# Kernel optimization log

Hardware: AMD Instinct MI355X
Metric: run time of the kernel (lower is better)

The kernel has to match this reference:

```python
import jax, jax.numpy as jnp
import numpy as np


def setup_inputs() -> dict:
    key = jax.random.key(0)
    k1, k2, k3, k4 = jax.random.split(key, 4)
    B, N, d_in, d_out = 8, 2048, 256, 256
    x = jax.random.normal(k1, (B, N, d_in), dtype=jnp.float32)
    adj_hat = jax.random.uniform(k2, (B, N, N), dtype=jnp.float32)
    W = jax.random.normal(k3, (d_out, d_in), dtype=jnp.float32) * (1.0 / np.sqrt(d_in))
    b = jax.random.normal(k4, (d_out,), dtype=jnp.float32) * 0.01
    return {"x": x, "adj_hat": adj_hat, "W": W, "b": b}


def reference(x, adj_hat, W, b):
    # Degrees from adj = adj_hat - I (i.e. without self loops): row sum minus diagonal.
    N = adj_hat.shape[1]
    diag = jnp.diagonal(adj_hat, axis1=-2, axis2=-1)          # [B, N]
    d = adj_hat.sum(axis=-1) - diag                           # [B, N]
    d_inv_sqrt = jnp.power(d, -0.5)                           # [B, N]
    # dad = D^-1/2 @ adj_hat @ D^-1/2  ==  d_i * a_ij * d_j (elementwise broadcast)
    dad = d_inv_sqrt[:, :, None] * adj_hat * d_inv_sqrt[:, None, :]  # [B, N, N]
    h = jnp.einsum('bnd,od->bno', x, W) + b                   # projection [B, N, d_out]
    return jnp.einsum('bnm,bmo->bno', dad, h)                 # [B, N, d_out]
```

## Files before the change

kernel.cpp:

```cpp
#include <hip/hip_runtime.h>
#include <hip/hip_bf16.h>


#define BATCH 8
#define NN    2048
#define DIN   256
#define DOUT  256
#define RTOT  (BATCH * NN)

typedef short  bf16x8  __attribute__((ext_vector_type(8)));
typedef short  short4v __attribute__((ext_vector_type(4)));
typedef float  f32x4   __attribute__((ext_vector_type(4)));

__device__ __forceinline__ short f2bf(float f) {
    union { float f; unsigned u; } v; v.f = f;
    unsigned r = v.u + 0x7fffu + ((v.u >> 16) & 1u);
    return (short)(r >> 16);
}

__global__ __launch_bounds__(256) void k_degree(const float* __restrict__ adj,
                                                float* __restrict__ dis) {
    int row = blockIdx.x;
    int b = row >> 11, n = row & (NN - 1);
    const float4* rp4 = (const float4*)(adj + ((size_t)b * NN + n) * NN);
    float s = 0.f;
#pragma unroll
    for (int i = 0; i < 2; i++) {
        float4 v = rp4[threadIdx.x + i * 256];
        s += (v.x + v.y) + (v.z + v.w);
    }
#pragma unroll
    for (int off = 32; off; off >>= 1) s += __shfl_down(s, off);
    __shared__ float red[4];
    if ((threadIdx.x & 63) == 0) red[threadIdx.x >> 6] = s;
    __syncthreads();
    if (threadIdx.x == 0) {
        float tot  = (red[0] + red[1]) + (red[2] + red[3]);
        float diag = ((const float*)rp4)[n];
        dis[row]   = rsqrtf(tot - diag);
    }
}

__global__ __launch_bounds__(256) void k_proj(const float* __restrict__ x,
                                              const float* __restrict__ W,
                                              const float* __restrict__ bias,
                                              const float* __restrict__ dis,
                                              unsigned short* __restrict__ hT) {
    const int mt  = blockIdx.y;
    const int nt  = blockIdx.x;
    const int tid = threadIdx.x;
    const int w = tid >> 6, lane = tid & 63;
    const int wr = w >> 1, wc = w & 1;
    const int l16 = lane & 15, quad = lane >> 4;

    __shared__ short As[128][32];
    __shared__ short Bs[128][32];

    f32x4 acc[4][4];
#pragma unroll
    for (int i = 0; i < 4; i++)
#pragma unroll
        for (int j = 0; j < 4; j++) acc[i][j] = (f32x4){0.f, 0.f, 0.f, 0.f};

    const float4* Wf4 = (const float4*)(W + (size_t)mt * 128 * DIN);
    const float4* Xf4 = (const float4*)(x + (size_t)nt * 128 * DIN);

    for (int kk = 0; kk < DIN / 32; kk++) {
        const int k0 = kk * 32;
        __syncthreads();
#pragma unroll
        for (int it = 0; it < 4; it++) {
            int idx = tid + it * 256;
            int r = idx >> 3, c = idx & 7;
            float4 va = Wf4[(size_t)r * (DIN / 4) + (k0 >> 2) + c];
            float4 vb = Xf4[(size_t)r * (DIN / 4) + (k0 >> 2) + c];
            short4v sa = { f2bf(va.x), f2bf(va.y), f2bf(va.z), f2bf(va.w) };
            short4v sb = { f2bf(vb.x), f2bf(vb.y), f2bf(vb.z), f2bf(vb.w) };
            *(short4v*)&As[r][c * 4] = sa;
            *(short4v*)&Bs[r][c * 4] = sb;
        }
        __syncthreads();
        bf16x8 af[4], bfv[4];
#pragma unroll
        for (int i = 0; i < 4; i++) af[i]  = *(bf16x8*)&As[wr * 64 + i * 16 + l16][quad * 8];
#pragma unroll
        for (int j = 0; j < 4; j++) bfv[j] = *(bf16x8*)&Bs[wc * 64 + j * 16 + l16][quad * 8];
#pragma unroll
        for (int i = 0; i < 4; i++)
#pragma unroll
            for (int j = 0; j < 4; j++)
                acc[i][j] = __builtin_amdgcn_mfma_f32_16x16x32_bf16(af[i], bfv[j], acc[i][j], 0, 0, 0);
    }

#pragma unroll
    for (int i = 0; i < 4; i++) {
        const int orow_base = mt * 128 + wr * 64 + i * 16 + quad * 4;
#pragma unroll
        for (int r = 0; r < 4; r++) {
            const int orow = orow_base + r;
            const float bb = bias[orow];
#pragma unroll
            for (int j = 0; j < 4; j++) {
                const int col = nt * 128 + wc * 64 + j * 16 + l16;
                float v = (acc[i][j][r] + bb) * dis[col];
                hT[(size_t)orow * RTOT + col] = (unsigned short)f2bf(v);
            }
        }
    }
}

__global__ __launch_bounds__(256) void k_main(const float* __restrict__ adj,
                                              const unsigned short* __restrict__ hT,
                                              const float* __restrict__ dis,
                                              float* __restrict__ out) {
    const int b     = blockIdx.x & 7;
    const int mtile = blockIdx.x >> 3;
    const int n0    = mtile * 64;
    const int tid = threadIdx.x;
    const int w = tid >> 6, lane = tid & 63;
    const int l16 = lane & 15, quad = lane >> 4;

    __shared__ short As[64][32];
    __shared__ short Bs[256][32];

    f32x4 acc[4][4];
#pragma unroll
    for (int i = 0; i < 4; i++)
#pragma unroll
        for (int j = 0; j < 4; j++) acc[i][j] = (f32x4){0.f, 0.f, 0.f, 0.f};

    const float4* adj4 = (const float4*)(adj + ((size_t)b * NN + n0) * NN);
    const unsigned short* hTb = hT + (size_t)b * NN;

    for (int kk = 0; kk < NN / 32; kk++) {
        const int k0 = kk * 32;
        __syncthreads();
#pragma unroll
        for (int it = 0; it < 2; it++) {
            int idx = tid + it * 256;
            int r = idx >> 3, c = idx & 7;
            float4 v = adj4[(size_t)r * (NN / 4) + (k0 >> 2) + c];
            short4v sv = { f2bf(v.x), f2bf(v.y), f2bf(v.z), f2bf(v.w) };
            *(short4v*)&As[r][c * 4] = sv;
        }
#pragma unroll
        for (int it = 0; it < 4; it++) {
            int idx = tid + it * 256;
            int o = idx >> 2, c = idx & 3;
            bf16x8 hv = *(const bf16x8*)(hTb + (size_t)o * RTOT + k0 + c * 8);
            *(bf16x8*)&Bs[o][c * 8] = hv;
        }
        __syncthreads();
        bf16x8 af[4], bfv[4];
#pragma unroll
        for (int i = 0; i < 4; i++) af[i]  = *(bf16x8*)&As[i * 16 + l16][quad * 8];
#pragma unroll
        for (int j = 0; j < 4; j++) bfv[j] = *(bf16x8*)&Bs[w * 64 + j * 16 + l16][quad * 8];
#pragma unroll
        for (int i = 0; i < 4; i++)
#pragma unroll
            for (int j = 0; j < 4; j++)
                acc[i][j] = __builtin_amdgcn_mfma_f32_16x16x32_bf16(af[i], bfv[j], acc[i][j], 0, 0, 0);
    }

    const float* disb = dis + (size_t)b * NN;
#pragma unroll
    for (int i = 0; i < 4; i++) {
#pragma unroll
        for (int r = 0; r < 4; r++) {
            const int nrow = n0 + i * 16 + quad * 4 + r;
            const float dn = disb[nrow];
#pragma unroll
            for (int j = 0; j < 4; j++) {
                const int ocol = w * 64 + j * 16 + l16;
                out[((size_t)b * NN + nrow) * DOUT + ocol] = dn * acc[i][j][r];
            }
        }
    }
}

extern "C" void kernel_launch(void* const* d_in, const int* in_sizes, int n_in,
                              void* d_out, int out_size, void* d_ws, size_t ws_size,
                              hipStream_t stream) {
    const float* x    = (const float*)d_in[0];
    const float* adj  = (const float*)d_in[1];
    const float* W    = (const float*)d_in[2];
    const float* bias = (const float*)d_in[3];
    float* out = (float*)d_out;

    float* dis = (float*)d_ws;
    unsigned short* hT = (unsigned short*)((char*)d_ws + 65536);

    k_degree<<<RTOT, 256, 0, stream>>>(adj, dis);
    k_proj<<<dim3(128, 2), 256, 0, stream>>>(x, W, bias, dis, hT);
    k_main<<<256, 256, 0, stream>>>(adj, hT, dis, out);
}
```

Before: 281.2 us.

## Pre-convert adjacency to bf16 in degree pass; load MFMA operands directly from global

The degree kernel now also writes a bf16 copy of the adjacency matrix, so the main GEMM reads half the bytes and skips per-tile conversion. The main kernel drops LDS staging and barriers and loads MFMA fragments straight from global memory. It also splits the output columns across two tiles, giving 512 blocks with launch bounds allowing two blocks per CU. The cost is an extra 128 MB write in the degree pass and uncoalesced direct global fragment loads that rely on cache reuse.

After: 312.2 us. 11.0% more time.

```diff
diff --git a/kernel.cpp b/kernel.cpp
--- a/kernel.cpp
+++ b/kernel.cpp
@@ -18,23 +18,29 @@
     return (short)(r >> 16);
 }
 
-__global__ __launch_bounds__(256) void k_degree(const float* __restrict__ adj,
-                                                float* __restrict__ dis) {
-    int row = blockIdx.x;
-    int b = row >> 11, n = row & (NN - 1);
-    const float4* rp4 = (const float4*)(adj + ((size_t)b * NN + n) * NN);
+__global__ __launch_bounds__(256) void k_degree_cvt(const float* __restrict__ adj,
+                                                    float* __restrict__ dis,
+                                                    unsigned short* __restrict__ abf) {
+    const int row = blockIdx.x;
+    const int n = row & (NN - 1);
+    const int tid = threadIdx.x;
+    const float4* rp4 = (const float4*)(adj + (size_t)row * NN);
+    unsigned short* op = abf + (size_t)row * NN;
+
     float s = 0.f;
 #pragma unroll
     for (int i = 0; i < 2; i++) {
-        float4 v = rp4[threadIdx.x + i * 256];
+        float4 v = rp4[tid + i * 256];
         s += (v.x + v.y) + (v.z + v.w);
+        short4v sv = { f2bf(v.x), f2bf(v.y), f2bf(v.z), f2bf(v.w) };
+        *(short4v*)(op + 4 * (tid + i * 256)) = sv;
     }
 #pragma unroll
     for (int off = 32; off; off >>= 1) s += __shfl_down(s, off);
     __shared__ float red[4];
-    if ((threadIdx.x & 63) == 0) red[threadIdx.x >> 6] = s;
+    if ((tid & 63) == 0) red[tid >> 6] = s;
     __syncthreads();
-    if (threadIdx.x == 0) {
+    if (tid == 0) {
         float tot  = (red[0] + red[1]) + (red[2] + red[3]);
         float diag = ((const float*)rp4)[n];
         dis[row]   = rsqrtf(tot - diag);
@@ -109,57 +115,47 @@
     }
 }
 
-__global__ __launch_bounds__(256) void k_main(const float* __restrict__ adj,
-                                              const unsigned short* __restrict__ hT,
-                                              const float* __restrict__ dis,
-                                              float* __restrict__ out) {
-    const int b     = blockIdx.x & 7;
-    const int mtile = blockIdx.x >> 3;
+__global__ __launch_bounds__(256, 2) void k_main(const unsigned short* __restrict__ abf,
+                                                 const unsigned short* __restrict__ hT,
+                                                 const float* __restrict__ dis,
+                                                 float* __restrict__ out) {
+    const int bx    = blockIdx.x;
+    const int b     = bx & 7;
+    const int mtile = (bx >> 3) & 31;
+    const int ctile = bx >> 8;
     const int n0    = mtile * 64;
     const int tid = threadIdx.x;
     const int w = tid >> 6, lane = tid & 63;
     const int l16 = lane & 15, quad = lane >> 4;
+    const int o0 = ctile * 128 + w * 32;
 
-    __shared__ short As[64][32];
-    __shared__ short Bs[256][32];
+    const unsigned short* aP[4];
+#pragma unroll
+    for (int i = 0; i < 4; i++)
+        aP[i] = abf + ((size_t)b * NN + n0 + i * 16 + l16) * NN + quad * 8;
+    const unsigned short* bP[2];
+#pragma unroll
+    for (int j = 0; j < 2; j++)
+        bP[j] = hT + (size_t)(o0 + j * 16 + l16) * RTOT + b * NN + quad * 8;
 
-    f32x4 acc[4][4];
+    f32x4 acc[4][2];
 #pragma unroll
     for (int i = 0; i < 4; i++)
 #pragma unroll
-        for (int j = 0; j < 4; j++) acc[i][j] = (f32x4){0.f, 0.f, 0.f, 0.f};
+        for (int j = 0; j < 2; j++) acc[i][j] = (f32x4){0.f, 0.f, 0.f, 0.f};
 
-    const float4* adj4 = (const float4*)(adj + ((size_t)b * NN + n0) * NN);
-    const unsigned short* hTb = hT + (size_t)b * NN;
-
+#pragma unroll 4
     for (int kk = 0; kk < NN / 32; kk++) {
-        const int k0 = kk * 32;
-        __syncthreads();
+        const int ko = kk * 32;
+        bf16x8 af[4], bfv[2];
 #pragma unroll
-        for (int it = 0; it < 2; it++) {
-            int idx = tid + it * 256;
-            int r = idx >> 3, c = idx & 7;
-            float4 v = adj4[(size_t)r * (NN / 4) + (k0 >> 2) + c];
-            short4v sv = { f2bf(v.x), f2bf(v.y), f2bf(v.z), f2bf(v.w) };
-            *(short4v*)&As[r][c * 4] = sv;
-        }
+        for (int i = 0; i < 4; i++) af[i]  = *(const bf16x8*)(aP[i] + ko);
 #pragma unroll
-        for (int it = 0; it < 4; it++) {
-            int idx = tid + it * 256;
-            int o = idx >> 2, c = idx & 3;
-            bf16x8 hv = *(const bf16x8*)(hTb + (size_t)o * RTOT + k0 + c * 8);
-            *(bf16x8*)&Bs[o][c * 8] = hv;
-        }
-        __syncthreads();
-        bf16x8 af[4], bfv[4];
-#pragma unroll
-        for (int i = 0; i < 4; i++) af[i]  = *(bf16x8*)&As[i * 16 + l16][quad * 8];
-#pragma unroll
-        for (int j = 0; j < 4; j++) bfv[j] = *(bf16x8*)&Bs[w * 64 + j * 16 + l16][quad * 8];
+        for (int j = 0; j < 2; j++) bfv[j] = *(const bf16x8*)(bP[j] + ko);
 #pragma unroll
         for (int i = 0; i < 4; i++)
 #pragma unroll
-            for (int j = 0; j < 4; j++)
+            for (int j = 0; j < 2; j++)
                 acc[i][j] = __builtin_amdgcn_mfma_f32_16x16x32_bf16(af[i], bfv[j], acc[i][j], 0, 0, 0);
     }
 
@@ -171,8 +167,8 @@
             const int nrow = n0 + i * 16 + quad * 4 + r;
             const float dn = disb[nrow];
 #pragma unroll
-            for (int j = 0; j < 4; j++) {
-                const int ocol = w * 64 + j * 16 + l16;
+            for (int j = 0; j < 2; j++) {
+                const int ocol = o0 + j * 16 + l16;
                 out[((size_t)b * NN + nrow) * DOUT + ocol] = dn * acc[i][j][r];
             }
         }
@@ -189,9 +185,10 @@
     float* out = (float*)d_out;
 
     float* dis = (float*)d_ws;
-    unsigned short* hT = (unsigned short*)((char*)d_ws + 65536);
+    unsigned short* hT  = (unsigned short*)((char*)d_ws + 65536);
+    unsigned short* abf = (unsigned short*)((char*)d_ws + 65536 + (size_t)RTOT * DOUT * 2);
 
-    k_degree<<<RTOT, 256, 0, stream>>>(adj, dis);
+    k_degree_cvt<<<RTOT, 256, 0, stream>>>(adj, dis, abf);
     k_proj<<<dim3(128, 2), 256, 0, stream>>>(x, W, bias, dis, hT);
-    k_main<<<256, 256, 0, stream>>>(adj, hT, dis, out);
+    k_main<<<512, 256, 0, stream>>>(abf, hT, dis, out);
 }
```
